# Kernel optimization log

Measured on AMD Instinct MI355X. Metric: run time of the kernel, lower is better.

## Reference

```python
import jax, jax.numpy as jnp
import numpy as np

N, K, D = 131072, 1024, 128
COMMITMENT_COST = 0.25


def setup_inputs() -> dict:
    key = jax.random.key(0)
    k1, k2 = jax.random.split(key)
    c_input = jax.random.normal(k1, (N, D), dtype=jnp.float32)
    # nn.Embedding weight initialized N(0, 0.1)
    embedding_weight = jax.random.normal(k2, (K, D), dtype=jnp.float32) * 0.1
    return {"c_input": c_input, "embedding_weight": embedding_weight}


def reference(c_input, embedding_weight):
    distances = (
        jnp.sum(c_input ** 2, axis=1, keepdims=True)
        + jnp.sum(embedding_weight ** 2, axis=1)
        - 2.0 * jnp.matmul(c_input, embedding_weight.T)
    )
    encoding_indices = jnp.argmin(distances, axis=1)  # [N]
    encodings = jax.nn.one_hot(encoding_indices, K, dtype=c_input.dtype)  # [N, K]
    # one-hot @ weight == direct gather
    quantized = embedding_weight[encoding_indices]  # [N, D]
    e_latent_loss = jnp.mean((jax.lax.stop_gradient(quantized) - c_input) ** 2)
    q_latent_loss = jnp.mean((quantized - jax.lax.stop_gradient(c_input)) ** 2)
    loss = q_latent_loss + COMMITMENT_COST * e_latent_loss
    # straight-through estimator
    quantized_st = c_input + jax.lax.stop_gradient(quantized - c_input)
    return (loss, quantized_st, encodings)
```

## Files before the change

### kernel.cpp

```cpp
#include <hip/hip_runtime.h>
#include <hip/hip_bf16.h>

#define NROWS 131072
#define KC 1024
#define DD 128
#define MARGIN 1e-3f

typedef __attribute__((ext_vector_type(8))) short short8;
typedef __attribute__((ext_vector_type(4))) float f32x4;

__device__ inline short f2bf_hi(float f) {
  unsigned u = __builtin_bit_cast(unsigned, f);
  u += 0x7fffu + ((u >> 16) & 1u);
  return (short)(u >> 16);
}
__device__ inline float bf2f(short s) {
  unsigned u = ((unsigned)(unsigned short)s) << 16;
  return __builtin_bit_cast(float, u);
}

__global__ void vq_prep(const float* __restrict__ E, short* __restrict__ EH,
                        short* __restrict__ EL, float* __restrict__ SE,
                        float* __restrict__ out) {
  int b = blockIdx.x, t = threadIdx.x;
  if (b < 64) {
    int idx = b * 256 + t;
    int s = (idx >> 6) & 3, l = idx & 63;
    int c = idx >> 8;
    int q = l >> 4, n = l & 15;
    const float* src = E + (16 * c + n) * DD + 32 * s + 8 * q;
    short8 h, lo;
#pragma unroll
    for (int j = 0; j < 8; ++j) {
      float x = src[j];
      short hb = f2bf_hi(x);
      h[j] = hb;
      lo[j] = f2bf_hi(x - bf2f(hb));
    }
    *(short8*)(EH + idx * 8) = h;
    *(short8*)(EL + idx * 8) = lo;
  } else {
    if (t == 0) out[0] = 0.f;
    for (int k = t; k < KC; k += 256) {
      double acc = 0.0;
      const float* er = E + k * DD;
      for (int i = 0; i < DD; ++i) { double v = (double)er[i]; acc += v * v; }
      SE[k] = (float)acc;
    }
  }
}

__global__ __launch_bounds__(256, 4) void vq_main(
    const float* __restrict__ X, const float* __restrict__ E,
    const short* __restrict__ EH, const short* __restrict__ EL,
    const float* __restrict__ SE, float* __restrict__ out) {
  __shared__ __align__(16) short lbh[8192];
  __shared__ __align__(16) short lbl[8192];
  __shared__ __align__(16) float lse[KC];
  __shared__ int lidx[128];
  __shared__ int lflag[128];
  __shared__ int lany;
  __shared__ float lx[128];
  __shared__ float lrv[4];
  __shared__ int lri[4];
  __shared__ float lsx;
  __shared__ float lloss[4];

  const int tid = threadIdx.x;
  const int w = tid >> 6, l = tid & 63, q = l >> 4, n = l & 15;
  const int row_base = blockIdx.x * 128;
  const int rot = blockIdx.x & 15;
  if (tid == 0) lany = 0;
  *(f32x4*)(lse + tid * 4) = *(const f32x4*)(SE + tid * 4);

  short8 ah[2][4], al[2][4];
#pragma unroll
  for (int mt = 0; mt < 2; ++mt) {
    const float* xp = X + (row_base + 32 * w + 16 * mt + n) * DD + 8 * q;
#pragma unroll
    for (int s = 0; s < 4; ++s) {
      f32x4 x0 = *(const f32x4*)(xp + 32 * s);
      f32x4 x1 = *(const f32x4*)(xp + 32 * s + 4);
#pragma unroll
      for (int j = 0; j < 4; ++j) {
        short hb = f2bf_hi(x0[j]);
        ah[mt][s][j] = hb;
        al[mt][s][j] = f2bf_hi(x0[j] - bf2f(hb));
        short hb2 = f2bf_hi(x1[j]);
        ah[mt][s][j + 4] = hb2;
        al[mt][s][j + 4] = f2bf_hi(x1[j] - bf2f(hb2));
      }
    }
  }

  float bestv[8], secv[8];
  int besti[8];
#pragma unroll
  for (int i = 0; i < 8; ++i) { bestv[i] = -3e38f; secv[i] = -3e38f; besti[i] = 0; }

  for (int cc = 0; cc < 16; ++cc) {
    const int ccr = (cc + rot) & 15;
    {
      const short8* gh = (const short8*)(EH + ccr * 8192);
      const short8* gl = (const short8*)(EL + ccr * 8192);
      short8* dh = (short8*)lbh;
      short8* dl = (short8*)lbl;
#pragma unroll
      for (int i = 0; i < 4; ++i) {
        int u = i * 256 + tid;
        dh[u] = gh[u];
        dl[u] = gl[u];
      }
    }
    __syncthreads();

    f32x4 acc[2][4];
#pragma unroll
    for (int mt = 0; mt < 2; ++mt)
#pragma unroll
      for (int nt = 0; nt < 4; ++nt) acc[mt][nt] = (f32x4){0.f, 0.f, 0.f, 0.f};

#pragma unroll
    for (int nt = 0; nt < 4; ++nt) {
#pragma unroll
      for (int s = 0; s < 4; ++s) {
        short8 bh  = *(const short8*)(lbh + ((nt * 4 + s) * 64 + l) * 8);
        short8 blo = *(const short8*)(lbl + ((nt * 4 + s) * 64 + l) * 8);
        acc[0][nt] = __builtin_amdgcn_mfma_f32_16x16x32_bf16(ah[0][s], bh,  acc[0][nt], 0, 0, 0);
        acc[1][nt] = __builtin_amdgcn_mfma_f32_16x16x32_bf16(ah[1][s], bh,  acc[1][nt], 0, 0, 0);
        acc[0][nt] = __builtin_amdgcn_mfma_f32_16x16x32_bf16(al[0][s], bh,  acc[0][nt], 0, 0, 0);
        acc[1][nt] = __builtin_amdgcn_mfma_f32_16x16x32_bf16(al[1][s], bh,  acc[1][nt], 0, 0, 0);
        acc[0][nt] = __builtin_amdgcn_mfma_f32_16x16x32_bf16(ah[0][s], blo, acc[0][nt], 0, 0, 0);
        acc[1][nt] = __builtin_amdgcn_mfma_f32_16x16x32_bf16(ah[1][s], blo, acc[1][nt], 0, 0, 0);
      }
    }
    __syncthreads();

#pragma unroll
    for (int nt = 0; nt < 4; ++nt) {
      int k = ccr * 64 + nt * 16 + n;
      float hse = 0.5f * lse[k];
#pragma unroll
      for (int mt = 0; mt < 2; ++mt)
#pragma unroll
        for (int r = 0; r < 4; ++r) {
          float sc = acc[mt][nt][r] - hse;
          int slot = mt * 4 + r;
          bool gt = sc > bestv[slot];
          secv[slot] = gt ? bestv[slot] : fmaxf(secv[slot], sc);
          if (gt) { bestv[slot] = sc; besti[slot] = k; }
        }
    }
  }

#pragma unroll
  for (int slot = 0; slot < 8; ++slot) {
    float v = bestv[slot], s2 = secv[slot];
    int bi = besti[slot];
#pragma unroll
    for (int m = 1; m <= 8; m <<= 1) {
      float v2 = __shfl_xor(v, m, 64);
      float sv2 = __shfl_xor(s2, m, 64);
      int i2 = __shfl_xor(bi, m, 64);
      float ns = fmaxf(fminf(v, v2), fmaxf(s2, sv2));
      if (v2 > v || (v2 == v && i2 < bi)) { v = v2; bi = i2; }
      s2 = ns;
    }
    if (n == 0) {
      int mt = slot >> 2, r = slot & 3;
      int rl = 32 * w + 16 * mt + 4 * q + r;
      int f = (v - s2) <= MARGIN;
      lidx[rl] = bi;
      lflag[rl] = f;
      if (f) lany = 1;
    }
  }
  __syncthreads();

  if (lany) {
    for (int rl = 0; rl < 128; ++rl) {
      if (lflag[rl] == 0) continue;
      if (tid < DD) lx[tid] = X[(row_base + rl) * DD + tid];
      __syncthreads();
      if (tid < 64) {
        double v0 = lx[tid], v1 = lx[tid + 64];
        double s = v0 * v0 + v1 * v1;
#pragma unroll
        for (int m = 1; m < 64; m <<= 1) s += __shfl_xor(s, m, 64);
        if (tid == 0) lsx = (float)s;
      }
      __syncthreads();
      float dmin = 3e38f; int kmin = 0;
      for (int kk = tid; kk < KC; kk += 256) {
        double dot = 0.0;
        const float* er = E + kk * DD;
        for (int i = 0; i < DD; ++i) dot += (double)lx[i] * (double)er[i];
        float a = lsx + lse[kk];
        float b2 = (float)(2.0 * dot);
        float dnp = a - b2;
        if (dnp < dmin) { dmin = dnp; kmin = kk; }
      }
#pragma unroll
      for (int m = 1; m < 64; m <<= 1) {
        float v2 = __shfl_xor(dmin, m, 64);
        int k2 = __shfl_xor(kmin, m, 64);
        if (v2 < dmin || (v2 == dmin && k2 < kmin)) { dmin = v2; kmin = k2; }
      }
      if (l == 0) { lrv[w] = dmin; lri[w] = kmin; }
      __syncthreads();
      if (tid == 0) {
        float dm = lrv[0]; int km = lri[0];
#pragma unroll
        for (int t2 = 1; t2 < 4; ++t2)
          if (lrv[t2] < dm || (lrv[t2] == dm && lri[t2] < km)) { dm = lrv[t2]; km = lri[t2]; }
        lidx[rl] = km;
      }
      __syncthreads();
    }
  }
  __syncthreads();

  float lp = 0.f;
  const int encb = 1 + NROWS * DD;
  for (int rl = w; rl < 128; rl += 4) {
    int row = row_base + rl;
    int idx = lidx[rl];
    float x0 = X[row * DD + l];
    float x1 = X[row * DD + 64 + l];
    float e0 = E[idx * DD + l];
    float e1 = E[idx * DD + 64 + l];
    float d0 = e0 - x0, d1 = e1 - x1;
    __builtin_nontemporal_store(x0 + d0, out + 1 + row * DD + l);
    __builtin_nontemporal_store(x1 + d1, out + 1 + row * DD + 64 + l);
    lp += d0 * d0 + d1 * d1;
    float* ob = out + encb + row * KC;
    if (l < 3) __builtin_nontemporal_store((l == idx) ? 1.f : 0.f, ob + l);
    for (int c = l; c < 255; c += 64) {
      int eb = 3 + 4 * c;
      f32x4 v;
      v[0] = (eb     == idx) ? 1.f : 0.f;
      v[1] = (eb + 1 == idx) ? 1.f : 0.f;
      v[2] = (eb + 2 == idx) ? 1.f : 0.f;
      v[3] = (eb + 3 == idx) ? 1.f : 0.f;
      __builtin_nontemporal_store(v, (f32x4*)(ob + eb));
    }
    if (l == 63) __builtin_nontemporal_store((1023 == idx) ? 1.f : 0.f, ob + 1023);
  }
#pragma unroll
  for (int m = 1; m < 64; m <<= 1) lp += __shfl_xor(lp, m, 64);
  if (l == 0) lloss[w] = lp;
  __syncthreads();
  if (tid == 0) {
    float t = (lloss[0] + lloss[1] + lloss[2] + lloss[3]) *
              (1.25f / ((float)NROWS * (float)DD));
    atomicAdd(out, t);
  }
}

extern "C" void kernel_launch(void* const* d_in, const int* in_sizes, int n_in,
                              void* d_out, int out_size, void* d_ws, size_t ws_size,
                              hipStream_t stream) {
  const float* X = (const float*)d_in[0];
  const float* E = (const float*)d_in[1];
  float* out = (float*)d_out;
  short* EH = (short*)d_ws;
  short* EL = EH + KC * DD;
  float* SE = (float*)(EL + KC * DD);
  vq_prep<<<65, 256, 0, stream>>>(E, EH, EL, SE, out);
  vq_main<<<NROWS / 128, 256, 0, stream>>>(X, E, EH, EL, SE, out);
}
```

Measured before the change: 832.2 us.

## Interleave one-hot zero stores with MFMA loop and scatter ones afterwards

The zero-fill of each block's one-hot encoding tile is spread across the 16 codebook chunk iterations, so the 512MB write stream overlaps the MFMA distance computation instead of following it. At the end only the single 1.0 per row is written with a normal store. The per-nt accumulate-then-argmin is also fused, which cuts the live accumulator registers. The risk is ordering: a nontemporal zero store and the later normal 1.0 store to the same address from different threads must become visible in program order.

Result: slower. 2.253 ms (+170.7%).

```diff
diff --git a/kernel.cpp b/kernel.cpp
--- a/kernel.cpp
+++ b/kernel.cpp
@@ -70,8 +70,14 @@
   const int w = tid >> 6, l = tid & 63, q = l >> 4, n = l & 15;
   const int row_base = blockIdx.x * 128;
   const int rot = blockIdx.x & 15;
+  const int encb = 1 + NROWS * DD;
   if (tid == 0) lany = 0;
   *(f32x4*)(lse + tid * 4) = *(const f32x4*)(SE + tid * 4);
+
+  float* zb = out + encb + row_base * KC;
+  if (tid < 3) __builtin_nontemporal_store(0.f, zb + tid);
+  else if (tid == 3) __builtin_nontemporal_store(0.f, zb + 131071);
+  float* zb4 = zb + 3;
 
   short8 ah[2][4], al[2][4];
 #pragma unroll
@@ -98,6 +104,7 @@
 #pragma unroll
   for (int i = 0; i < 8; ++i) { bestv[i] = -3e38f; secv[i] = -3e38f; besti[i] = 0; }
 
+  const f32x4 z4 = {0.f, 0.f, 0.f, 0.f};
   for (int cc = 0; cc < 16; ++cc) {
     const int ccr = (cc + rot) & 15;
     {
@@ -114,43 +121,49 @@
     }
     __syncthreads();
 
-    f32x4 acc[2][4];
-#pragma unroll
-    for (int mt = 0; mt < 2; ++mt)
-#pragma unroll
-      for (int nt = 0; nt < 4; ++nt) acc[mt][nt] = (f32x4){0.f, 0.f, 0.f, 0.f};
+    {
+      int jb = cc * 2048 + tid * 8;
+#pragma unroll
+      for (int u2 = 0; u2 < 8; ++u2) {
+        int j = jb + u2;
+        if (j < 32767) __builtin_nontemporal_store(z4, (f32x4*)(zb4 + 4 * j));
+      }
+    }
 
 #pragma unroll
     for (int nt = 0; nt < 4; ++nt) {
+      f32x4 a0 = {0.f, 0.f, 0.f, 0.f}, a1 = {0.f, 0.f, 0.f, 0.f};
 #pragma unroll
       for (int s = 0; s < 4; ++s) {
         short8 bh  = *(const short8*)(lbh + ((nt * 4 + s) * 64 + l) * 8);
         short8 blo = *(const short8*)(lbl + ((nt * 4 + s) * 64 + l) * 8);
-        acc[0][nt] = __builtin_amdgcn_mfma_f32_16x16x32_bf16(ah[0][s], bh,  acc[0][nt], 0, 0, 0);
-        acc[1][nt] = __builtin_amdgcn_mfma_f32_16x16x32_bf16(ah[1][s], bh,  acc[1][nt], 0, 0, 0);
-        acc[0][nt] = __builtin_amdgcn_mfma_f32_16x16x32_bf16(al[0][s], bh,  acc[0][nt], 0, 0, 0);
-        acc[1][nt] = __builtin_amdgcn_mfma_f32_16x16x32_bf16(al[1][s], bh,  acc[1][nt], 0, 0, 0);
-        acc[0][nt] = __builtin_amdgcn_mfma_f32_16x16x32_bf16(ah[0][s], blo, acc[0][nt], 0, 0, 0);
-        acc[1][nt] = __builtin_amdgcn_mfma_f32_16x16x32_bf16(ah[1][s], blo, acc[1][nt], 0, 0, 0);
-      }
-    }
-    __syncthreads();
-
-#pragma unroll
-    for (int nt = 0; nt < 4; ++nt) {
+        a0 = __builtin_amdgcn_mfma_f32_16x16x32_bf16(ah[0][s], bh,  a0, 0, 0, 0);
+        a1 = __builtin_amdgcn_mfma_f32_16x16x32_bf16(ah[1][s], bh,  a1, 0, 0, 0);
+        a0 = __builtin_amdgcn_mfma_f32_16x16x32_bf16(al[0][s], bh,  a0, 0, 0, 0);
+        a1 = __builtin_amdgcn_mfma_f32_16x16x32_bf16(al[1][s], bh,  a1, 0, 0, 0);
+        a0 = __builtin_amdgcn_mfma_f32_16x16x32_bf16(ah[0][s], blo, a0, 0, 0, 0);
+        a1 = __builtin_amdgcn_mfma_f32_16x16x32_bf16(ah[1][s], blo, a1, 0, 0, 0);
+      }
       int k = ccr * 64 + nt * 16 + n;
       float hse = 0.5f * lse[k];
 #pragma unroll
-      for (int mt = 0; mt < 2; ++mt)
-#pragma unroll
-        for (int r = 0; r < 4; ++r) {
-          float sc = acc[mt][nt][r] - hse;
-          int slot = mt * 4 + r;
-          bool gt = sc > bestv[slot];
-          secv[slot] = gt ? bestv[slot] : fmaxf(secv[slot], sc);
-          if (gt) { bestv[slot] = sc; besti[slot] = k; }
+      for (int r = 0; r < 4; ++r) {
+        {
+          float sc = a0[r] - hse;
+          bool gt = sc > bestv[r];
+          secv[r] = gt ? bestv[r] : fmaxf(secv[r], sc);
+          if (gt) { bestv[r] = sc; besti[r] = k; }
         }
-    }
+        {
+          int sl = 4 + r;
+          float sc = a1[r] - hse;
+          bool gt = sc > bestv[sl];
+          secv[sl] = gt ? bestv[sl] : fmaxf(secv[sl], sc);
+          if (gt) { bestv[sl] = sc; besti[sl] = k; }
+        }
+      }
+    }
+    __syncthreads();
   }
 
 #pragma unroll
@@ -221,7 +234,6 @@
   __syncthreads();
 
   float lp = 0.f;
-  const int encb = 1 + NROWS * DD;
   for (int rl = w; rl < 128; rl += 4) {
     int row = row_base + rl;
     int idx = lidx[rl];
@@ -233,18 +245,7 @@
     __builtin_nontemporal_store(x0 + d0, out + 1 + row * DD + l);
     __builtin_nontemporal_store(x1 + d1, out + 1 + row * DD + 64 + l);
     lp += d0 * d0 + d1 * d1;
-    float* ob = out + encb + row * KC;
-    if (l < 3) __builtin_nontemporal_store((l == idx) ? 1.f : 0.f, ob + l);
-    for (int c = l; c < 255; c += 64) {
-      int eb = 3 + 4 * c;
-      f32x4 v;
-      v[0] = (eb     == idx) ? 1.f : 0.f;
-      v[1] = (eb + 1 == idx) ? 1.f : 0.f;
-      v[2] = (eb + 2 == idx) ? 1.f : 0.f;
-      v[3] = (eb + 3 == idx) ? 1.f : 0.f;
-      __builtin_nontemporal_store(v, (f32x4*)(ob + eb));
-    }
-    if (l == 63) __builtin_nontemporal_store((1023 == idx) ? 1.f : 0.f, ob + 1023);
+    if (l == (idx & 63)) out[encb + row * KC + idx] = 1.f;
   }
 #pragma unroll
   for (int m = 1; m < 64; m <<= 1) lp += __shfl_xor(lp, m, 64);
```
